# Kernel optimization log

Hardware: AMD Instinct MI355X
Metric: run time of the kernel (lower is better)

Reference implementation:

```python
import jax, jax.numpy as jnp
import numpy as np

N = 1048576            # num nodes == num edges (required by the original's indexing)
C = 64                 # in_channels
FIRST = N // 3         # analogue of the hardcoded 8-of-24 fixed-weight prefix


def setup_inputs() -> dict:
    key = jax.random.key(0)
    k1, k2, k3 = jax.random.split(key, 3)
    x = jax.random.normal(k1, (N, C), dtype=jnp.float32)
    edge_index = jax.random.randint(k2, (2, N), 0, N, dtype=jnp.int64)
    # EdgeWeightLayer.lin : Linear(in_channels -> out_channels*heads = 1)
    lin_w = jax.random.normal(k3, (1, C), dtype=jnp.float32) / np.float32(np.sqrt(C))
    lin_b = jnp.zeros((1,), dtype=jnp.float32)
    w1 = jnp.array([1.0], dtype=jnp.float32)    # fixed_edge_weights_1
    w2 = jnp.array([-0.5], dtype=jnp.float32)   # learnable_edge_weights_2
    w3 = jnp.array([1.5], dtype=jnp.float32)    # learnable_edge_weights_3
    return {"x": x, "lin_w": lin_w, "lin_b": lin_b, "w1": w1, "w2": w2, "w3": w3,
            "edge_index": edge_index}


def reference(x, lin_w, lin_b, w1, w2, w3, edge_index):
    n = x.shape[0]
    # --- EdgeWeightLayer: add self loops, message = lin(x_j - x_i), aggr='add' at target i
    loop = jnp.arange(n, dtype=edge_index.dtype)
    src = jnp.concatenate([edge_index[0], loop])   # j
    dst = jnp.concatenate([edge_index[1], loop])   # i
    msg = (x[src] - x[dst]) @ lin_w.T + lin_b      # [2N, 1]
    learned = jax.ops.segment_sum(msg, dst, num_segments=n)  # [n, 1] per-node scores

    # --- final_edge_scores construction (generalized 24 -> N, 8 -> FIRST)
    idx = jnp.arange(n)
    base = jnp.where(idx < FIRST, w1[0],
                     jnp.where((idx - FIRST) % 2 == 0, w2[0], w3[0]))
    scores = base[:, None] + jnp.where(idx >= FIRST, learned[:, 0], 0.0)[:, None]  # [n,1]

    # --- per-edge gather -> scalar scale -> scatter-add (the explicit loop in torch)
    e = edge_index.shape[1]
    agg = jax.ops.segment_sum(x[edge_index[0]] * scores[:e],
                              edge_index[1], num_segments=n)   # [n, C]
    return jax.nn.relu(agg)
```

## Files before the change

kernel.cpp:

```cpp
#include <hip/hip_runtime.h>

#define C 64

typedef float fx4 __attribute__((ext_vector_type(4)));

__global__ void dot_hist_kernel(const float4* __restrict__ x4,
                                const float4* __restrict__ w4,
                                const int* __restrict__ ei,
                                float* __restrict__ d,
                                int* __restrict__ count,
                                int* __restrict__ rank,
                                int n) {
    int gtid = blockIdx.x * blockDim.x + threadIdx.x;

    if (gtid < n) {
        int t = ei[n + gtid];
        rank[gtid] = atomicAdd(&count[t], 1);
    }

    int wave = gtid >> 6;
    int lane = threadIdx.x & 63;
    int sub  = lane >> 4;
    int sl   = lane & 15;
    int node = wave * 4 + sub;
    if (node >= n) return;
    float4 v = x4[(size_t)node * 16 + sl];
    float4 w = w4[sl];
    float t = v.x * w.x + v.y * w.y + v.z * w.z + v.w * w.w;
    t += __shfl_xor(t, 8, 64);
    t += __shfl_xor(t, 4, 64);
    t += __shfl_xor(t, 2, 64);
    t += __shfl_xor(t, 1, 64);
    if (sl == 0) d[node] = t;
}

__global__ void scatter_scan1_kernel(const int* __restrict__ ei,
                                     const float* __restrict__ d,
                                     const float* __restrict__ lin_b,
                                     float* __restrict__ learned,
                                     const int* __restrict__ count,
                                     int* __restrict__ off,
                                     int* __restrict__ partial,
                                     int n, int first) {
    __shared__ int sh[256];
    int tid = threadIdx.x;
    int gid = blockIdx.x * 256 + tid;

    int t = ei[n + gid];
    if (t >= first) {
        int s = ei[gid];
        atomicAdd(&learned[t], d[s] - d[t] + lin_b[0]);
    }

    int v = count[gid];
    sh[tid] = v;
    __syncthreads();
    for (int o = 1; o < 256; o <<= 1) {
        int tt = (tid >= o) ? sh[tid - o] : 0;
        __syncthreads();
        sh[tid] += tt;
        __syncthreads();
    }
    off[gid] = sh[tid] - v;
    if (tid == 255) partial[blockIdx.x] = sh[255];
}

__global__ void scan2_kernel(int* __restrict__ partial, int nb) {
    __shared__ int sh[256];
    int tid = threadIdx.x;
    int chunk = nb / 256;
    int base = tid * chunk;
    int sum = 0;
    for (int k = 0; k < chunk; ++k) sum += partial[base + k];
    sh[tid] = sum;
    __syncthreads();
    for (int o = 1; o < 256; o <<= 1) {
        int t = (tid >= o) ? sh[tid - o] : 0;
        __syncthreads();
        sh[tid] += t;
        __syncthreads();
    }
    int running = sh[tid] - sum;
    for (int k = 0; k < chunk; ++k) {
        int v = partial[base + k];
        partial[base + k] = running;
        running += v;
    }
}

__global__ void reorder_kernel(const int* __restrict__ ei,
                               const float* __restrict__ learned,
                               const int* __restrict__ off,
                               const int* __restrict__ partial,
                               const int* __restrict__ rank,
                               int2* __restrict__ srcscore,
                               const float* __restrict__ lin_b,
                               const float* __restrict__ w1,
                               const float* __restrict__ w2,
                               const float* __restrict__ w3,
                               int n, int first) {
    int e = blockIdx.x * blockDim.x + threadIdx.x;
    if (e >= n) return;
    float score;
    if (e < first) {
        score = w1[0];
    } else {
        float base = (((e - first) & 1) == 0) ? w2[0] : w3[0];
        score = base + lin_b[0] + learned[e];
    }
    int s = ei[e];
    int t = ei[n + e];
    int pos = off[t] + partial[t >> 8] + rank[e];
    srcscore[pos] = make_int2(s, __float_as_int(score));
}

__global__ void gather_kernel(const float4* __restrict__ x4,
                              const int* __restrict__ off,
                              const int* __restrict__ partial,
                              const int2* __restrict__ srcscore,
                              float4* __restrict__ out4, int n) {
    int gtid = blockIdx.x * blockDim.x + threadIdx.x;
    int wave = gtid >> 6;
    int lane = threadIdx.x & 63;
    int sub  = lane >> 4;
    int sl   = lane & 15;
    int node = wave * 4 + sub;
    if (node >= n) return;
    int beg = off[node] + partial[node >> 8];
    int end = (node + 1 < n) ? (off[node + 1] + partial[(node + 1) >> 8]) : n;
    float4 acc = make_float4(0.f, 0.f, 0.f, 0.f);
    int base = sub << 4;
    for (int j0 = beg; j0 < end; j0 += 16) {
        int rem = end - j0;
        int m = (rem < 16) ? rem : 16;
        int2 p = make_int2(0, 0);
        if (sl < m) p = srcscore[j0 + sl];
        for (int k = 0; k < m; ++k) {
            int   src = __shfl(p.x, base + k, 64);
            float s   = __int_as_float(__shfl(p.y, base + k, 64));
            float4 v = x4[(size_t)src * 16 + sl];
            acc.x += v.x * s;
            acc.y += v.y * s;
            acc.z += v.z * s;
            acc.w += v.w * s;
        }
    }
    acc.x = fmaxf(acc.x, 0.f);
    acc.y = fmaxf(acc.y, 0.f);
    acc.z = fmaxf(acc.z, 0.f);
    acc.w = fmaxf(acc.w, 0.f);
    fx4 av;
    av.x = acc.x; av.y = acc.y; av.z = acc.z; av.w = acc.w;
    __builtin_nontemporal_store(av, (fx4*)&out4[(size_t)node * 16 + sl]);
}

extern "C" void kernel_launch(void* const* d_in, const int* in_sizes, int n_in,
                              void* d_out, int out_size, void* d_ws, size_t ws_size,
                              hipStream_t stream) {
    const float* x     = (const float*)d_in[0];
    const float* lin_w = (const float*)d_in[1];
    const float* lin_b = (const float*)d_in[2];
    const float* w1    = (const float*)d_in[3];
    const float* w2    = (const float*)d_in[4];
    const float* w3    = (const float*)d_in[5];
    const int*   ei    = (const int*)d_in[6];
    float* out = (float*)d_out;

    const int n = in_sizes[0] / C;
    const int first = n / 3;
    const int nb = n / 256;

    float* d_dot    = (float*)d_ws;
    float* learned  = d_dot + n;
    int*   count    = (int*)(learned + n);
    int*   off      = count + n;
    int*   rank     = off + n;
    int2*  srcscore = (int2*)(rank + n);
    int*   partial  = (int*)(srcscore + n);

    hipMemsetAsync(learned, 0, (size_t)2 * n * sizeof(int), stream);

    dot_hist_kernel<<<dim3(n / 16), dim3(256), 0, stream>>>(
        (const float4*)x, (const float4*)lin_w, ei, d_dot, count, rank, n);
    scatter_scan1_kernel<<<dim3(nb), dim3(256), 0, stream>>>(
        ei, d_dot, lin_b, learned, count, off, partial, n, first);
    scan2_kernel<<<dim3(1), dim3(256), 0, stream>>>(partial, nb);
    reorder_kernel<<<dim3(nb), dim3(256), 0, stream>>>(ei, learned, off, partial,
                                                       rank, srcscore, lin_b,
                                                       w1, w2, w3, n, first);
    gather_kernel<<<dim3(n / 16), dim3(256), 0, stream>>>(
        (const float4*)x, off, partial, srcscore, (float4*)out, n);
}
```

Before: 635.2 us.

## Drop rank array and fold self-loop terms into per-node count algebra

Result: slower. 657.7 us (+3.5%).

```diff
diff --git a/kernel.cpp b/kernel.cpp
--- a/kernel.cpp
+++ b/kernel.cpp
@@ -9,13 +9,12 @@
                                 const int* __restrict__ ei,
                                 float* __restrict__ d,
                                 int* __restrict__ count,
-                                int* __restrict__ rank,
                                 int n) {
     int gtid = blockIdx.x * blockDim.x + threadIdx.x;
 
     if (gtid < n) {
         int t = ei[n + gtid];
-        rank[gtid] = atomicAdd(&count[t], 1);
+        atomicAdd(&count[t], 1);
     }
 
     int wave = gtid >> 6;
@@ -36,8 +35,7 @@
 
 __global__ void scatter_scan1_kernel(const int* __restrict__ ei,
                                      const float* __restrict__ d,
-                                     const float* __restrict__ lin_b,
-                                     float* __restrict__ learned,
+                                     float* __restrict__ sumd,
                                      const int* __restrict__ count,
                                      int* __restrict__ off,
                                      int* __restrict__ partial,
@@ -49,7 +47,7 @@
     int t = ei[n + gid];
     if (t >= first) {
         int s = ei[gid];
-        atomicAdd(&learned[t], d[s] - d[t] + lin_b[0]);
+        atomicAdd(&sumd[t], d[s]);
     }
 
     int v = count[gid];
@@ -89,10 +87,11 @@
 }
 
 __global__ void reorder_kernel(const int* __restrict__ ei,
-                               const float* __restrict__ learned,
-                               const int* __restrict__ off,
+                               const float* __restrict__ sumd,
+                               const float* __restrict__ d,
+                               const int* __restrict__ count,
+                               int* __restrict__ off,
                                const int* __restrict__ partial,
-                               const int* __restrict__ rank,
                                int2* __restrict__ srcscore,
                                const float* __restrict__ lin_b,
                                const float* __restrict__ w1,
@@ -106,11 +105,12 @@
         score = w1[0];
     } else {
         float base = (((e - first) & 1) == 0) ? w2[0] : w3[0];
-        score = base + lin_b[0] + learned[e];
+        float cnt = (float)count[e];
+        score = base + sumd[e] - cnt * d[e] + (cnt + 1.0f) * lin_b[0];
     }
     int s = ei[e];
     int t = ei[n + e];
-    int pos = off[t] + partial[t >> 8] + rank[e];
+    int pos = partial[t >> 8] + atomicAdd(&off[t], 1);
     srcscore[pos] = make_int2(s, __float_as_int(score));
 }
 
@@ -126,8 +126,9 @@
     int sl   = lane & 15;
     int node = wave * 4 + sub;
     if (node >= n) return;
-    int beg = off[node] + partial[node >> 8];
-    int end = (node + 1 < n) ? (off[node + 1] + partial[(node + 1) >> 8]) : n;
+    int beg = partial[node >> 8] + ((node & 255) ? off[node - 1] : 0);
+    int np1 = node + 1;
+    int end = (np1 < n) ? (partial[np1 >> 8] + ((np1 & 255) ? off[node] : 0)) : n;
     float4 acc = make_float4(0.f, 0.f, 0.f, 0.f);
     int base = sub << 4;
     for (int j0 = beg; j0 < end; j0 += 16) {
@@ -171,23 +172,22 @@
     const int nb = n / 256;
 
     float* d_dot    = (float*)d_ws;
-    float* learned  = d_dot + n;
-    int*   count    = (int*)(learned + n);
+    float* sumd     = d_dot + n;
+    int*   count    = (int*)(sumd + n);
     int*   off      = count + n;
-    int*   rank     = off + n;
-    int2*  srcscore = (int2*)(rank + n);
+    int2*  srcscore = (int2*)(off + n);
     int*   partial  = (int*)(srcscore + n);
 
-    hipMemsetAsync(learned, 0, (size_t)2 * n * sizeof(int), stream);
+    hipMemsetAsync(sumd, 0, (size_t)2 * n * sizeof(int), stream);
 
     dot_hist_kernel<<<dim3(n / 16), dim3(256), 0, stream>>>(
-        (const float4*)x, (const float4*)lin_w, ei, d_dot, count, rank, n);
+        (const float4*)x, (const float4*)lin_w, ei, d_dot, count, n);
     scatter_scan1_kernel<<<dim3(nb), dim3(256), 0, stream>>>(
-        ei, d_dot, lin_b, learned, count, off, partial, n, first);
+        ei, d_dot, sumd, count, off, partial, n, first);
     scan2_kernel<<<dim3(1), dim3(256), 0, stream>>>(partial, nb);
-    reorder_kernel<<<dim3(nb), dim3(256), 0, stream>>>(ei, learned, off, partial,
-                                                       rank, srcscore, lin_b,
-                                                       w1, w2, w3, n, first);
+    reorder_kernel<<<dim3(nb), dim3(256), 0, stream>>>(ei, sumd, d_dot, count,
+                                                       off, partial, srcscore,
+                                                       lin_b, w1, w2, w3, n, first);
     gather_kernel<<<dim3(n / 16), dim3(256), 0, stream>>>(
         (const float4*)x, off, partial, srcscore, (float4*)out, n);
 }
```
